# Optimization experiments

Measured on AMD Instinct MI355X. Metric: run time of the kernel, lower is better.

Reference implementation:

```python
import jax, jax.numpy as jnp
import numpy as np

# ---- static config (mirrors SRNNConfig) ----
N = 2048          # num_units
N_E = N // 2      # excitatory
N_I = N - N_E     # inhibitory
N_A = 3           # n_a_E = n_a_I (SFA timescales per neuron)
H = 0.04
UNFOLDS = 6
DT = H / UNFOLDS
IN_SIZE = 512
B = 512
STATE_SIZE = N_E * N_A + N_I * N_A + N_E + N_I + N  # 10240
SPARSITY = 0.5


def inv_softplus(x):
    return float(np.log(np.expm1(x)))


def piecewise_sigmoid(x, S_a=0.9, S_c=0.0):
    """Bounded [0,1] activation: linear center, quadratic edges (matches torch source)."""
    a = S_a / 2.0
    c = S_c
    k = 0.5 / (1.0 - 2.0 * a)  # = 5.0 for S_a=0.9
    x1 = c + a - 1.0
    x2 = c - a
    x3 = c + a
    x4 = c + 1.0 - a
    quad_rise = k * (x - x1) * (x - x1)
    linear = x - c + 0.5
    quad_cap = 1.0 - k * (x - x4) * (x - x4)
    out = jnp.where(x < x1, jnp.zeros_like(x), quad_rise)
    out = jnp.where(x >= x2, linear, out)
    out = jnp.where(x > x3, quad_cap, out)
    out = jnp.where(x > x4, jnp.ones_like(x), out)
    return out


def setup_inputs() -> dict:
    key = jax.random.key(0)
    ks = jax.random.split(key, 6)
    f32 = jnp.float32
    W_raw = (jax.random.normal(ks[0], (N, N)) * np.sqrt(2.0 / N)).astype(f32)
    sparsity_mask = (jax.random.uniform(ks[1], (N, N)) > SPARSITY).astype(f32)
    W_raw = W_raw * sparsity_mask  # W_init masked as in __init__
    W_in = (jax.random.normal(ks[2], (N, IN_SIZE)) * 0.1).astype(f32)
    a_0 = jnp.full((N,), 0.35, f32)
    log_tau_d = jnp.full((1,), inv_softplus(0.1), f32)
    log_tau_a_E_lo = jnp.full((1, 1), inv_softplus(0.25), f32)
    log_tau_a_E_hi = jnp.full((1, 1), inv_softplus(10.0), f32)
    log_c_E = jnp.full((1, N_A), -3.0, f32)
    c_0_E = jnp.zeros((1, N_A), f32)
    log_tau_a_I_lo = jnp.full((1, 1), inv_softplus(0.25), f32)
    log_tau_a_I_hi = jnp.full((1, 1), inv_softplus(10.0), f32)
    log_c_I = jnp.full((1, N_A), -3.0, f32)
    c_0_I = jnp.zeros((1, N_A), f32)
    log_tau_b_rec_E = jnp.full((1,), inv_softplus(1.0), f32)
    log_tau_b_rel_E = jnp.full((1,), inv_softplus(0.25), f32)
    log_tau_b_rec_I = jnp.full((1,), inv_softplus(1.0), f32)
    log_tau_b_rel_I = jnp.full((1,), inv_softplus(0.25), f32)
    u = jax.random.normal(ks[3], (B, IN_SIZE), f32)
    state = jax.random.normal(ks[4], (B, STATE_SIZE), f32) * 0.1
    return {
        "W_raw": W_raw, "W_in": W_in, "sparsity_mask": sparsity_mask, "a_0": a_0,
        "log_tau_d": log_tau_d,
        "log_tau_a_E_lo": log_tau_a_E_lo, "log_tau_a_E_hi": log_tau_a_E_hi,
        "log_c_E": log_c_E, "c_0_E": c_0_E,
        "log_tau_a_I_lo": log_tau_a_I_lo, "log_tau_a_I_hi": log_tau_a_I_hi,
        "log_c_I": log_c_I, "c_0_I": c_0_I,
        "log_tau_b_rec_E": log_tau_b_rec_E, "log_tau_b_rel_E": log_tau_b_rel_E,
        "log_tau_b_rec_I": log_tau_b_rec_I, "log_tau_b_rel_I": log_tau_b_rel_I,
        "u": u, "state": state,
    }


def reference(W_raw, W_in, sparsity_mask, a_0, log_tau_d,
              log_tau_a_E_lo, log_tau_a_E_hi, log_c_E, c_0_E,
              log_tau_a_I_lo, log_tau_a_I_hi, log_c_I, c_0_I,
              log_tau_b_rec_E, log_tau_b_rel_E, log_tau_b_rec_I, log_tau_b_rel_I,
              u, state):
    sp = jax.nn.softplus
    # ---- unpack flat state: [a_E, a_I, b_E, b_I, x] ----
    i = 0
    a_E = state[:, i:i + N_E * N_A].reshape(-1, N_E, N_A); i += N_E * N_A
    a_I = state[:, i:i + N_I * N_A].reshape(-1, N_I, N_A); i += N_I * N_A
    b_E = state[:, i:i + N_E]; i += N_E
    b_I = state[:, i:i + N_I]; i += N_I
    x = state[:, i:i + N]

    # ---- effective weights (Dale's law: E cols +, I cols -) + sparsity ----
    W_pos = sp(W_raw)
    sign = jnp.concatenate([jnp.ones((N_E,), W_raw.dtype), -jnp.ones((N_I,), W_raw.dtype)])
    W_eff = W_pos * sign[None, :] * sparsity_mask  # (N, N)

    # ---- time constants / coefficients ----
    tau_d = sp(log_tau_d)                              # (1,)
    t = jnp.linspace(0.0, 1.0, N_A).astype(x.dtype)
    tau_a_E = sp(log_tau_a_E_lo) + (sp(log_tau_a_E_hi) - sp(log_tau_a_E_lo)) * t  # (1, N_A)
    tau_a_I = sp(log_tau_a_I_lo) + (sp(log_tau_a_I_hi) - sp(log_tau_a_I_lo)) * t
    c_E = sp(log_c_E)                                  # (1, N_A)
    c_I = sp(log_c_I)
    tau_b_rec_E = sp(log_tau_b_rec_E); tau_b_rel_E = sp(log_tau_b_rel_E)
    tau_b_rec_I = sp(log_tau_b_rec_I); tau_b_rel_I = sp(log_tau_b_rel_I)

    I_ext = u @ W_in.T + a_0[None, :]                  # (B, N), constant over sub-steps

    g_x = DT / tau_d                                   # (1,)
    g_aE = DT / tau_a_E[None]                          # (1, 1, N_A)
    g_aI = DT / tau_a_I[None]

    for _ in range(UNFOLDS):
        # adaptation-shifted membrane potential
        x_eff_E = x[:, :N_E] - (a_E * c_E[None]).sum(-1)   # (B, N_E)
        x_eff_I = x[:, N_E:] - (a_I * c_I[None]).sum(-1)   # (B, N_I)
        r = piecewise_sigmoid(jnp.concatenate([x_eff_E, x_eff_I], axis=-1))  # (B, N)
        r_E, r_I = r[:, :N_E], r[:, N_E:]
        # synaptic depression gates the transmitted rates
        r_dep = jnp.concatenate([b_E * r_E, b_I * r_I], axis=-1)
        I_syn = r_dep @ W_eff.T + I_ext                    # (B, N)
        # ---- semi-implicit Euler sub-step ----
        x = (x + g_x * I_syn) / (1.0 + g_x)
        a_E = (a_E + g_aE * (r_E[:, :, None] + c_0_E[None])) / (1.0 + g_aE)
        a_I = (a_I + g_aI * (r_I[:, :, None] + c_0_I[None])) / (1.0 + g_aI)
        b_E = (b_E + DT / tau_b_rec_E) / (1.0 + DT / tau_b_rec_E + DT * r_E / tau_b_rel_E)
        b_I = (b_I + DT / tau_b_rec_I) / (1.0 + DT / tau_b_rec_I + DT * r_I / tau_b_rel_I)

    batch = state.shape[0]
    new_state = jnp.concatenate(
        [a_E.reshape(batch, -1), a_I.reshape(batch, -1), b_E, b_I, x], axis=-1)
    return new_state
```

## Files before the change

### kernel.cpp

```cpp
#include <hip/hip_runtime.h>
#include <math.h>

#define N_TOT 2048
#define NE    1024
#define BATCH 512
#define IN_SZ 512
#define SS    10240
#define AI_OFF 3072
#define BE_OFF 6144
#define BI_OFF 7168
#define X_OFF  8192

typedef __attribute__((ext_vector_type(8))) short bf16x8;
typedef __attribute__((ext_vector_type(4))) float f32x4;


__device__ __forceinline__ float sp_f(float x) {
    return fmaxf(x, 0.f) + log1pf(expf(-fabsf(x)));
}

__device__ __forceinline__ float psig(float x) {
    if (x >= -0.45f) {
        if (x <= 0.45f) return x + 0.5f;
        if (x > 0.55f)  return 1.f;
        float d = x - 0.55f;
        return 1.f - 5.f * d * d;
    }
    if (x < -0.55f) return 0.f;
    float d = x + 0.55f;
    return 5.f * d * d;
}

__device__ __forceinline__ ushort f2bf(float f) {
    unsigned u = __float_as_uint(f);
    unsigned r = (u + 0x7fffu + ((u >> 16) & 1u)) >> 16;
    return (ushort)r;
}

__device__ __forceinline__ void gload16(const void* g, void* l) {
    __builtin_amdgcn_global_load_lds(
        (const __attribute__((address_space(1))) void*)g,
        (__attribute__((address_space(3))) void*)l, 16, 0, 0);
}

__global__ void k_params(const float* ltd, const float* loE, const float* hiE,
                         const float* lcE, const float* c0E,
                         const float* loI, const float* hiI,
                         const float* lcI, const float* c0I,
                         const float* recE, const float* relE,
                         const float* recI, const float* relI,
                         float* __restrict__ P) {
    if (threadIdx.x == 0 && blockIdx.x == 0) {
        const float DTf = (float)(0.04 / 6.0);
        float gx = DTf / sp_f(ltd[0]);
        P[0] = gx;
        P[29] = 1.f / (1.f + gx);
        float sElo = sp_f(loE[0]), sEhi = sp_f(hiE[0]);
        float sIlo = sp_f(loI[0]), sIhi = sp_f(hiI[0]);
        for (int j = 0; j < 3; ++j) {
            float t = 0.5f * (float)j;
            float gE = DTf / (sElo + (sEhi - sElo) * t);
            float gI = DTf / (sIlo + (sIhi - sIlo) * t);
            P[1 + j] = gE;  P[23 + j] = 1.f / (1.f + gE);
            P[4 + j] = gI;  P[26 + j] = 1.f / (1.f + gI);
            P[7 + j]  = sp_f(lcE[j]);
            P[10 + j] = sp_f(lcI[j]);
            P[13 + j] = c0E[j];
            P[16 + j] = c0I[j];
        }
        P[19] = DTf / sp_f(recE[0]);
        P[20] = DTf / sp_f(relE[0]);
        P[21] = DTf / sp_f(recI[0]);
        P[22] = DTf / sp_f(relI[0]);
    }
}

__global__ __launch_bounds__(256) void k_weff(const float* __restrict__ Wr,
                                              const float* __restrict__ mask,
                                              ushort* __restrict__ We) {
    int i = blockIdx.x * 256 + threadIdx.x;
    float4 w = ((const float4*)Wr)[i];
    float4 m = ((const float4*)mask)[i];
    int col = (i * 4) & (N_TOT - 1);
    float s = (col < NE) ? 1.f : -1.f;
    ushort4 o;
    o.x = f2bf(sp_f(w.x) * m.x * s);
    o.y = f2bf(sp_f(w.y) * m.y * s);
    o.z = f2bf(sp_f(w.z) * m.z * s);
    o.w = f2bf(sp_f(w.w) * m.w * s);
    ((ushort4*)We)[i] = o;
}

__global__ __launch_bounds__(256) void k_cvt(const float* __restrict__ in,
                                             ushort* __restrict__ out) {
    int i = blockIdx.x * 256 + threadIdx.x;
    float4 v = ((const float4*)in)[i];
    ushort4 o;
    o.x = f2bf(v.x); o.y = f2bf(v.y); o.z = f2bf(v.z); o.w = f2bf(v.w);
    ((ushort4*)out)[i] = o;
}

__global__ __launch_bounds__(256) void k_r_first(const float* __restrict__ st,
                                                 const float* __restrict__ P,
                                                 float* __restrict__ r_ws,
                                                 ushort* __restrict__ rdep) {
    int idx = blockIdx.x * 256 + threadIdx.x;
    int m = idx >> 11, n = idx & (N_TOT - 1);
    const float* row = st + (size_t)m * SS;
    bool isE = n < NE;
    int na = isE ? n : n - NE;
    const float* a = row + (isE ? 0 : AI_OFF) + 3 * na;
    const float* c = P + (isE ? 7 : 10);
    float x = row[X_OFF + n];
    float xeff = x - (a[0] * c[0] + a[1] * c[1] + a[2] * c[2]);
    float r = psig(xeff);
    float bb = row[isE ? (BE_OFF + n) : (BI_OFF + na)];
    r_ws[idx] = r;
    rdep[idx] = f2bf(bb * r);
}

template<int EPI, bool CALC_R>
__global__ __launch_bounds__(256)
void mgemm(const ushort* __restrict__ A, const ushort* __restrict__ Bt, int K,
           const float* __restrict__ a0,
           const float* __restrict__ Iext,
           float* __restrict__ outIext,
           float* __restrict__ stateOut,
           const float* __restrict__ P,
           float* __restrict__ r_ws,
           ushort* __restrict__ rdep_out) {
    __shared__ __align__(16) ushort lds[2][2][64 * 32];
    const int tid = threadIdx.x;
    const int bm = blockIdx.y * 64;
    const int bn = blockIdx.x * 64;
    const int wv = tid >> 6;
    const int lane = tid & 63;
    const int wr = wv >> 1, wc = wv & 1;

    const int srow = tid >> 2;
    const int sc = tid & 3;
    const int gk = (sc ^ ((srow >> 1) & 3)) * 8;
    const ushort* gA = A + (size_t)(bm + srow) * K + gk;
    const ushort* gB = Bt + (size_t)(bn + srow) * K + gk;

    int aoff[2], boff[2];
    {
        const int kc = lane >> 4;
        const int rr = lane & 15;
#pragma unroll
        for (int i = 0; i < 2; ++i) {
            int r = wr * 32 + i * 16 + rr;
            aoff[i] = r * 64 + ((kc ^ ((r >> 1) & 3)) << 4);
        }
#pragma unroll
        for (int j = 0; j < 2; ++j) {
            int r = wc * 32 + j * 16 + rr;
            boff[j] = r * 64 + ((kc ^ ((r >> 1) & 3)) << 4);
        }
    }

    f32x4 acc[2][2];
#pragma unroll
    for (int i = 0; i < 2; ++i)
#pragma unroll
        for (int j = 0; j < 2; ++j)
            acc[i][j] = f32x4{0.f, 0.f, 0.f, 0.f};

    gload16(gA, (char*)&lds[0][0][0] + wv * 1024);
    gload16(gB, (char*)&lds[0][1][0] + wv * 1024);
    __syncthreads();

    const int nsteps = K >> 5;
    int cur = 0;
    for (int s = 0; s < nsteps; ++s) {
        if (s + 1 < nsteps) {
            gload16(gA + (s + 1) * 32, (char*)&lds[cur ^ 1][0][0] + wv * 1024);
            gload16(gB + (s + 1) * 32, (char*)&lds[cur ^ 1][1][0] + wv * 1024);
        }
        const char* At = (const char*)&lds[cur][0][0];
        const char* Bl = (const char*)&lds[cur][1][0];
        bf16x8 af0 = *(const bf16x8*)(At + aoff[0]);
        bf16x8 af1 = *(const bf16x8*)(At + aoff[1]);
        bf16x8 bg0 = *(const bf16x8*)(Bl + boff[0]);
        bf16x8 bg1 = *(const bf16x8*)(Bl + boff[1]);
        acc[0][0] = __builtin_amdgcn_mfma_f32_16x16x32_bf16(af0, bg0, acc[0][0], 0, 0, 0);
        acc[0][1] = __builtin_amdgcn_mfma_f32_16x16x32_bf16(af0, bg1, acc[0][1], 0, 0, 0);
        acc[1][0] = __builtin_amdgcn_mfma_f32_16x16x32_bf16(af1, bg0, acc[1][0], 0, 0, 0);
        acc[1][1] = __builtin_amdgcn_mfma_f32_16x16x32_bf16(af1, bg1, acc[1][1], 0, 0, 0);
        __syncthreads();
        cur ^= 1;
    }

    if (EPI == 0) {
#pragma unroll
        for (int i = 0; i < 2; ++i) {
#pragma unroll
            for (int j = 0; j < 2; ++j) {
                int m0 = bm + wr * 32 + i * 16 + (lane >> 4) * 4;
                int n = bn + wc * 32 + j * 16 + (lane & 15);
                float av = a0[n];
#pragma unroll
                for (int q = 0; q < 4; ++q)
                    outIext[(m0 + q) * N_TOT + n] = acc[i][j][q] + av;
            }
        }
    } else {
        const float gx = P[0];
        const float inv1gx = P[29];
#pragma unroll
        for (int i = 0; i < 2; ++i) {
#pragma unroll
            for (int j = 0; j < 2; ++j) {
                int m0 = bm + wr * 32 + i * 16 + (lane >> 4) * 4;
                int n = bn + wc * 32 + j * 16 + (lane & 15);
                bool isE = n < NE;
                int na = isE ? n : n - NE;
                const float* ga = P + (isE ? 1 : 4);
                const float* iga = P + (isE ? 23 : 26);
                const float* c0 = P + (isE ? 13 : 16);
                const float* cc = P + (isE ? 7 : 10);
                float kbrec = isE ? P[19] : P[21];
                float kbrel = isE ? P[20] : P[22];
                int aofs = (isE ? 0 : AI_OFF) + 3 * na;
                int bofs = isE ? (BE_OFF + n) : (BI_OFF + na);
#pragma unroll
                for (int q = 0; q < 4; ++q) {
                    int m = m0 + q;
                    float* row = stateOut + (size_t)m * SS;
                    int idx = m * N_TOT + n;
                    float Isyn = acc[i][j][q] + Iext[idx];
                    float x = row[X_OFF + n];
                    float xn = (x + gx * Isyn) * inv1gx;
                    row[X_OFF + n] = xn;

                    float r = r_ws[idx];
                    float* a = row + aofs;
                    float av0 = (a[0] + ga[0] * (r + c0[0])) * iga[0];
                    float av1 = (a[1] + ga[1] * (r + c0[1])) * iga[1];
                    float av2 = (a[2] + ga[2] * (r + c0[2])) * iga[2];
                    a[0] = av0; a[1] = av1; a[2] = av2;

                    float bb = row[bofs];
                    bb = (bb + kbrec) / (1.f + kbrec + kbrel * r);
                    row[bofs] = bb;

                    if (CALC_R) {
                        float xeff = xn - (av0 * cc[0] + av1 * cc[1] + av2 * cc[2]);
                        float rn = psig(xeff);
                        r_ws[idx] = rn;
                        rdep_out[idx] = f2bf(bb * rn);
                    }
                }
            }
        }
    }
}

extern "C" void kernel_launch(void* const* d_in, const int* in_sizes, int n_in,
                              void* d_out, int out_size, void* d_ws, size_t ws_size,
                              hipStream_t stream) {
    const float* W_raw = (const float*)d_in[0];
    const float* W_in  = (const float*)d_in[1];
    const float* mask  = (const float*)d_in[2];
    const float* a_0   = (const float*)d_in[3];
    const float* ltd   = (const float*)d_in[4];
    const float* loE   = (const float*)d_in[5];
    const float* hiE   = (const float*)d_in[6];
    const float* lcE   = (const float*)d_in[7];
    const float* c0E   = (const float*)d_in[8];
    const float* loI   = (const float*)d_in[9];
    const float* hiI   = (const float*)d_in[10];
    const float* lcI   = (const float*)d_in[11];
    const float* c0I   = (const float*)d_in[12];
    const float* recE  = (const float*)d_in[13];
    const float* relE  = (const float*)d_in[14];
    const float* recI  = (const float*)d_in[15];
    const float* relI  = (const float*)d_in[16];
    const float* u     = (const float*)d_in[17];
    const float* state = (const float*)d_in[18];
    float* out = (float*)d_out;
    char* wsb = (char*)d_ws;

    ushort* We     = (ushort*)(wsb);
    float*  Iext   = (float*)(wsb + (8u << 20));
    float*  r_ws   = (float*)(wsb + (12u << 20));
    ushort* rdep0  = (ushort*)(wsb + (16u << 20));
    ushort* rdep1  = (ushort*)(wsb + (18u << 20));
    ushort* u_bf   = (ushort*)(wsb + (20u << 20));
    ushort* win_bf = (ushort*)(wsb + (21u << 20));
    float*  P      = (float*)(wsb + (23u << 20));

    hipMemcpyAsync(out, state, (size_t)BATCH * SS * sizeof(float),
                   hipMemcpyDeviceToDevice, stream);

    k_params<<<1, 64, 0, stream>>>(ltd, loE, hiE, lcE, c0E, loI, hiI, lcI, c0I,
                                   recE, relE, recI, relI, P);

    k_weff<<<(N_TOT * N_TOT / 4) / 256, 256, 0, stream>>>(W_raw, mask, We);
    k_cvt<<<(BATCH * IN_SZ / 4) / 256, 256, 0, stream>>>(u, u_bf);
    k_cvt<<<(N_TOT * IN_SZ / 4) / 256, 256, 0, stream>>>(W_in, win_bf);

    mgemm<0, false><<<dim3(N_TOT / 64, BATCH / 64), 256, 0, stream>>>(
        u_bf, win_bf, IN_SZ, a_0, nullptr, Iext, nullptr, nullptr, nullptr, nullptr);

    k_r_first<<<(BATCH * N_TOT) / 256, 256, 0, stream>>>(out, P, r_ws, rdep0);

    ushort* rbufs[2] = {rdep0, rdep1};
    for (int t = 0; t < 6; ++t) {
        ushort* rin  = rbufs[t & 1];
        ushort* rout = rbufs[(t + 1) & 1];
        if (t < 5)
            mgemm<1, true><<<dim3(N_TOT / 64, BATCH / 64), 256, 0, stream>>>(
                rin, We, N_TOT, nullptr, Iext, nullptr, out, P, r_ws, rout);
        else
            mgemm<1, false><<<dim3(N_TOT / 64, BATCH / 64), 256, 0, stream>>>(
                rin, We, N_TOT, nullptr, Iext, nullptr, out, P, r_ws, nullptr);
    }
}
```

Before: 374.9 us.

## Fuse input GEMM and all unfold steps into one persistent kernel with grid barrier

Replaces the separate input-projection GEMM, first-rate kernel and six per-step GEMM launches with one persistent kernel of 256 blocks. The blocks synchronise between sub-steps through an atomic global barrier. Each thread keeps its slice of x, a, b, r and I_ext in registers across all steps, and writes the state only once at the end. This drops the full-state device copy and the global Iext and r_ws round-trips. The K tile grows to 128 with a 512-thread block, at the cost of spin-barrier latency and a requirement that all 256 blocks are co-resident.

```diff
diff --git a/kernel.cpp b/kernel.cpp
--- a/kernel.cpp
+++ b/kernel.cpp
@@ -10,6 +10,8 @@
 #define BE_OFF 6144
 #define BI_OFF 7168
 #define X_OFF  8192
+#define NBLK  256
+#define LDS_B_OFF 16384
 
 typedef __attribute__((ext_vector_type(8))) short bf16x8;
 typedef __attribute__((ext_vector_type(4))) float f32x4;
@@ -43,14 +45,37 @@
         (__attribute__((address_space(3))) void*)l, 16, 0, 0);
 }
 
+__device__ __forceinline__ void gbar(unsigned* bar) {
+    __threadfence();
+    __syncthreads();
+    if (threadIdx.x == 0) {
+        unsigned* cnt = bar;
+        unsigned* gen = bar + 1;
+        unsigned g = __hip_atomic_load(gen, __ATOMIC_RELAXED, __HIP_MEMORY_SCOPE_AGENT);
+        unsigned a = __hip_atomic_fetch_add(cnt, 1u, __ATOMIC_ACQ_REL, __HIP_MEMORY_SCOPE_AGENT);
+        if (a == NBLK - 1) {
+            __hip_atomic_store(cnt, 0u, __ATOMIC_RELAXED, __HIP_MEMORY_SCOPE_AGENT);
+            __hip_atomic_fetch_add(gen, 1u, __ATOMIC_RELEASE, __HIP_MEMORY_SCOPE_AGENT);
+        } else {
+            while (__hip_atomic_load(gen, __ATOMIC_ACQUIRE, __HIP_MEMORY_SCOPE_AGENT) == g) {
+                __builtin_amdgcn_s_sleep(2);
+            }
+        }
+    }
+    __syncthreads();
+    __threadfence();
+}
+
 __global__ void k_params(const float* ltd, const float* loE, const float* hiE,
                          const float* lcE, const float* c0E,
                          const float* loI, const float* hiI,
                          const float* lcI, const float* c0I,
                          const float* recE, const float* relE,
                          const float* recI, const float* relI,
-                         float* __restrict__ P) {
+                         float* __restrict__ P, unsigned* __restrict__ bar) {
     if (threadIdx.x == 0 && blockIdx.x == 0) {
+        bar[0] = 0u;
+        bar[1] = 0u;
         const float DTf = (float)(0.04 / 6.0);
         float gx = DTf / sp_f(ltd[0]);
         P[0] = gx;
@@ -100,158 +125,181 @@
     ((ushort4*)out)[i] = o;
 }
 
-__global__ __launch_bounds__(256) void k_r_first(const float* __restrict__ st,
-                                                 const float* __restrict__ P,
-                                                 float* __restrict__ r_ws,
-                                                 ushort* __restrict__ rdep) {
-    int idx = blockIdx.x * 256 + threadIdx.x;
-    int m = idx >> 11, n = idx & (N_TOT - 1);
-    const float* row = st + (size_t)m * SS;
-    bool isE = n < NE;
-    int na = isE ? n : n - NE;
-    const float* a = row + (isE ? 0 : AI_OFF) + 3 * na;
-    const float* c = P + (isE ? 7 : 10);
-    float x = row[X_OFF + n];
-    float xeff = x - (a[0] * c[0] + a[1] * c[1] + a[2] * c[2]);
-    float r = psig(xeff);
-    float bb = row[isE ? (BE_OFF + n) : (BI_OFF + na)];
-    r_ws[idx] = r;
-    rdep[idx] = f2bf(bb * r);
-}
-
-template<int EPI, bool CALC_R>
-__global__ __launch_bounds__(256)
-void mgemm(const ushort* __restrict__ A, const ushort* __restrict__ Bt, int K,
-           const float* __restrict__ a0,
-           const float* __restrict__ Iext,
-           float* __restrict__ outIext,
-           float* __restrict__ stateOut,
-           const float* __restrict__ P,
-           float* __restrict__ r_ws,
-           ushort* __restrict__ rdep_out) {
-    __shared__ __align__(16) ushort lds[2][2][64 * 32];
-    const int tid = threadIdx.x;
-    const int bm = blockIdx.y * 64;
-    const int bn = blockIdx.x * 64;
-    const int wv = tid >> 6;
+__global__ __launch_bounds__(512, 2)
+void kfused(const ushort* __restrict__ We,
+            const ushort* __restrict__ u_bf,
+            const ushort* __restrict__ win_bf,
+            const float* __restrict__ a0,
+            const float* __restrict__ P,
+            const float* __restrict__ state_in,
+            float* __restrict__ state_out,
+            ushort* __restrict__ rdep0,
+            ushort* __restrict__ rdep1,
+            unsigned* __restrict__ bar) {
+    __shared__ __align__(16) ushort lds[2][16384];
+    const int tid  = threadIdx.x;
     const int lane = tid & 63;
-    const int wr = wv >> 1, wc = wv & 1;
-
-    const int srow = tid >> 2;
-    const int sc = tid & 3;
-    const int gk = (sc ^ ((srow >> 1) & 3)) * 8;
-    const ushort* gA = A + (size_t)(bm + srow) * K + gk;
-    const ushort* gB = Bt + (size_t)(bn + srow) * K + gk;
-
-    int aoff[2], boff[2];
+    const int wv   = tid >> 6;
+    const int wr   = wv >> 1;
+    const int wc   = wv & 1;
+    const int bn   = blockIdx.x * 64;
+    const int bm   = blockIdx.y * 64;
+
+    const int srow = tid >> 4;
+    const int sch  = tid & 15;
+    const int sgc  = sch ^ (srow & 7);
+
+    const int kc = lane >> 4, rr = lane & 15;
+    const int ar = wr * 16 + rr;
+    int aO[4], bO0[4], bO1[4];
     {
-        const int kc = lane >> 4;
-        const int rr = lane & 15;
-#pragma unroll
-        for (int i = 0; i < 2; ++i) {
-            int r = wr * 32 + i * 16 + rr;
-            aoff[i] = r * 64 + ((kc ^ ((r >> 1) & 3)) << 4);
-        }
+        const int br0 = wc * 32 + rr;
+        const int br1 = wc * 32 + 16 + rr;
+#pragma unroll
+        for (int s = 0; s < 4; ++s) {
+            aO[s]  = ar * 256 + (((s * 4 + kc) ^ (ar & 7)) << 4);
+            bO0[s] = LDS_B_OFF + br0 * 256 + (((s * 4 + kc) ^ (br0 & 7)) << 4);
+            bO1[s] = LDS_B_OFF + br1 * 256 + (((s * 4 + kc) ^ (br1 & 7)) << 4);
+        }
+    }
+
+    auto stage = [&](int buf, const ushort* A, const ushort* Bt, int K, int k0) {
+        char* Ld = (char*)&lds[buf][0];
+        const ushort* Ap  = A  + (size_t)(bm + srow) * K + k0 + sgc * 8;
+        const ushort* Ap2 = A  + (size_t)(bm + srow + 32) * K + k0 + sgc * 8;
+        const ushort* Bp  = Bt + (size_t)(bn + srow) * K + k0 + sgc * 8;
+        const ushort* Bp2 = Bt + (size_t)(bn + srow + 32) * K + k0 + sgc * 8;
+        gload16(Ap,  Ld + tid * 16);
+        gload16(Ap2, Ld + tid * 16 + 8192);
+        gload16(Bp,  Ld + LDS_B_OFF + tid * 16);
+        gload16(Bp2, Ld + LDS_B_OFF + tid * 16 + 8192);
+    };
+    auto compute = [&](int buf, f32x4* acc) {
+        const char* Ld = (const char*)&lds[buf][0];
+#pragma unroll
+        for (int s = 0; s < 4; ++s) {
+            bf16x8 af = *(const bf16x8*)(Ld + aO[s]);
+            bf16x8 b0 = *(const bf16x8*)(Ld + bO0[s]);
+            bf16x8 b1 = *(const bf16x8*)(Ld + bO1[s]);
+            acc[0] = __builtin_amdgcn_mfma_f32_16x16x32_bf16(af, b0, acc[0], 0, 0, 0);
+            acc[1] = __builtin_amdgcn_mfma_f32_16x16x32_bf16(af, b1, acc[1], 0, 0, 0);
+        }
+    };
+    auto gemmK = [&](const ushort* A, const ushort* Bt, int K, f32x4* acc) {
+        const int nkt = K >> 7;
+        stage(0, A, Bt, K, 0);
+        __syncthreads();
+        for (int kt = 0; kt < nkt; ++kt) {
+            int cur = kt & 1;
+            if (kt + 1 < nkt) stage(cur ^ 1, A, Bt, K, (kt + 1) << 7);
+            compute(cur, acc);
+            __syncthreads();
+        }
+    };
+
+    const float gx = P[0], inv1gx = P[29];
+    const int mbase = bm + wr * 16 + (lane >> 4) * 4;
+    int nj[2], aofs[2], bofs[2];
+    float ga[2][3], iga[2][3], c0v[2][3], ccv[2][3], kbrecv[2], kbrelv[2];
+#pragma unroll
+    for (int j = 0; j < 2; ++j) {
+        int n = bn + wc * 32 + j * 16 + (lane & 15);
+        nj[j] = n;
+        bool isE = n < NE;
+        int na = isE ? n : n - NE;
+#pragma unroll
+        for (int c = 0; c < 3; ++c) {
+            ga[j][c]  = P[(isE ? 1 : 4) + c];
+            iga[j][c] = P[(isE ? 23 : 26) + c];
+            c0v[j][c] = P[(isE ? 13 : 16) + c];
+            ccv[j][c] = P[(isE ? 7 : 10) + c];
+        }
+        kbrecv[j] = isE ? P[19] : P[21];
+        kbrelv[j] = isE ? P[20] : P[22];
+        aofs[j] = (isE ? 0 : AI_OFF) + 3 * na;
+        bofs[j] = isE ? (BE_OFF + n) : (BI_OFF + na);
+    }
+
+    f32x4 acc[2];
+    acc[0] = f32x4{0.f, 0.f, 0.f, 0.f};
+    acc[1] = f32x4{0.f, 0.f, 0.f, 0.f};
+    gemmK(u_bf, win_bf, IN_SZ, acc);
+
+    float iext[2][4], xs[2][4], as[2][4][3], bs[2][4], rs[2][4];
+#pragma unroll
+    for (int j = 0; j < 2; ++j) {
+        float a0v = a0[nj[j]];
+#pragma unroll
+        for (int q = 0; q < 4; ++q) iext[j][q] = acc[j][q] + a0v;
+    }
+
+#pragma unroll
+    for (int j = 0; j < 2; ++j) {
+#pragma unroll
+        for (int q = 0; q < 4; ++q) {
+            int m = mbase + q;
+            const float* row = state_in + (size_t)m * SS;
+            float xv  = row[X_OFF + nj[j]];
+            float av0 = row[aofs[j] + 0];
+            float av1 = row[aofs[j] + 1];
+            float av2 = row[aofs[j] + 2];
+            float bv  = row[bofs[j]];
+            xs[j][q] = xv;
+            as[j][q][0] = av0; as[j][q][1] = av1; as[j][q][2] = av2;
+            bs[j][q] = bv;
+            float xeff = xv - (av0 * ccv[j][0] + av1 * ccv[j][1] + av2 * ccv[j][2]);
+            float rv = psig(xeff);
+            rs[j][q] = rv;
+            rdep0[(size_t)m * N_TOT + nj[j]] = f2bf(bv * rv);
+        }
+    }
+    gbar(bar);
+
+    ushort* rin  = rdep0;
+    ushort* rout = rdep1;
+    for (int t = 0; t < 6; ++t) {
+        acc[0] = f32x4{0.f, 0.f, 0.f, 0.f};
+        acc[1] = f32x4{0.f, 0.f, 0.f, 0.f};
+        gemmK(rin, We, N_TOT, acc);
 #pragma unroll
         for (int j = 0; j < 2; ++j) {
-            int r = wc * 32 + j * 16 + rr;
-            boff[j] = r * 64 + ((kc ^ ((r >> 1) & 3)) << 4);
-        }
-    }
-
-    f32x4 acc[2][2];
-#pragma unroll
-    for (int i = 0; i < 2; ++i)
-#pragma unroll
-        for (int j = 0; j < 2; ++j)
-            acc[i][j] = f32x4{0.f, 0.f, 0.f, 0.f};
-
-    gload16(gA, (char*)&lds[0][0][0] + wv * 1024);
-    gload16(gB, (char*)&lds[0][1][0] + wv * 1024);
-    __syncthreads();
-
-    const int nsteps = K >> 5;
-    int cur = 0;
-    for (int s = 0; s < nsteps; ++s) {
-        if (s + 1 < nsteps) {
-            gload16(gA + (s + 1) * 32, (char*)&lds[cur ^ 1][0][0] + wv * 1024);
-            gload16(gB + (s + 1) * 32, (char*)&lds[cur ^ 1][1][0] + wv * 1024);
-        }
-        const char* At = (const char*)&lds[cur][0][0];
-        const char* Bl = (const char*)&lds[cur][1][0];
-        bf16x8 af0 = *(const bf16x8*)(At + aoff[0]);
-        bf16x8 af1 = *(const bf16x8*)(At + aoff[1]);
-        bf16x8 bg0 = *(const bf16x8*)(Bl + boff[0]);
-        bf16x8 bg1 = *(const bf16x8*)(Bl + boff[1]);
-        acc[0][0] = __builtin_amdgcn_mfma_f32_16x16x32_bf16(af0, bg0, acc[0][0], 0, 0, 0);
-        acc[0][1] = __builtin_amdgcn_mfma_f32_16x16x32_bf16(af0, bg1, acc[0][1], 0, 0, 0);
-        acc[1][0] = __builtin_amdgcn_mfma_f32_16x16x32_bf16(af1, bg0, acc[1][0], 0, 0, 0);
-        acc[1][1] = __builtin_amdgcn_mfma_f32_16x16x32_bf16(af1, bg1, acc[1][1], 0, 0, 0);
-        __syncthreads();
-        cur ^= 1;
-    }
-
-    if (EPI == 0) {
-#pragma unroll
-        for (int i = 0; i < 2; ++i) {
-#pragma unroll
-            for (int j = 0; j < 2; ++j) {
-                int m0 = bm + wr * 32 + i * 16 + (lane >> 4) * 4;
-                int n = bn + wc * 32 + j * 16 + (lane & 15);
-                float av = a0[n];
-#pragma unroll
-                for (int q = 0; q < 4; ++q)
-                    outIext[(m0 + q) * N_TOT + n] = acc[i][j][q] + av;
-            }
-        }
-    } else {
-        const float gx = P[0];
-        const float inv1gx = P[29];
-#pragma unroll
-        for (int i = 0; i < 2; ++i) {
-#pragma unroll
-            for (int j = 0; j < 2; ++j) {
-                int m0 = bm + wr * 32 + i * 16 + (lane >> 4) * 4;
-                int n = bn + wc * 32 + j * 16 + (lane & 15);
-                bool isE = n < NE;
-                int na = isE ? n : n - NE;
-                const float* ga = P + (isE ? 1 : 4);
-                const float* iga = P + (isE ? 23 : 26);
-                const float* c0 = P + (isE ? 13 : 16);
-                const float* cc = P + (isE ? 7 : 10);
-                float kbrec = isE ? P[19] : P[21];
-                float kbrel = isE ? P[20] : P[22];
-                int aofs = (isE ? 0 : AI_OFF) + 3 * na;
-                int bofs = isE ? (BE_OFF + n) : (BI_OFF + na);
-#pragma unroll
-                for (int q = 0; q < 4; ++q) {
-                    int m = m0 + q;
-                    float* row = stateOut + (size_t)m * SS;
-                    int idx = m * N_TOT + n;
-                    float Isyn = acc[i][j][q] + Iext[idx];
-                    float x = row[X_OFF + n];
-                    float xn = (x + gx * Isyn) * inv1gx;
-                    row[X_OFF + n] = xn;
-
-                    float r = r_ws[idx];
-                    float* a = row + aofs;
-                    float av0 = (a[0] + ga[0] * (r + c0[0])) * iga[0];
-                    float av1 = (a[1] + ga[1] * (r + c0[1])) * iga[1];
-                    float av2 = (a[2] + ga[2] * (r + c0[2])) * iga[2];
-                    a[0] = av0; a[1] = av1; a[2] = av2;
-
-                    float bb = row[bofs];
-                    bb = (bb + kbrec) / (1.f + kbrec + kbrel * r);
-                    row[bofs] = bb;
-
-                    if (CALC_R) {
-                        float xeff = xn - (av0 * cc[0] + av1 * cc[1] + av2 * cc[2]);
-                        float rn = psig(xeff);
-                        r_ws[idx] = rn;
-                        rdep_out[idx] = f2bf(bb * rn);
-                    }
+#pragma unroll
+            for (int q = 0; q < 4; ++q) {
+                float Isyn = acc[j][q] + iext[j][q];
+                float xn = (xs[j][q] + gx * Isyn) * inv1gx;
+                xs[j][q] = xn;
+                float rv = rs[j][q];
+                float an0 = (as[j][q][0] + ga[j][0] * (rv + c0v[j][0])) * iga[j][0];
+                float an1 = (as[j][q][1] + ga[j][1] * (rv + c0v[j][1])) * iga[j][1];
+                float an2 = (as[j][q][2] + ga[j][2] * (rv + c0v[j][2])) * iga[j][2];
+                as[j][q][0] = an0; as[j][q][1] = an1; as[j][q][2] = an2;
+                float bnv = (bs[j][q] + kbrecv[j]) /
+                            (1.f + kbrecv[j] + kbrelv[j] * rv);
+                bs[j][q] = bnv;
+                if (t < 5) {
+                    float xeff = xn - (an0 * ccv[j][0] + an1 * ccv[j][1] + an2 * ccv[j][2]);
+                    float rn = psig(xeff);
+                    rs[j][q] = rn;
+                    rout[(size_t)(mbase + q) * N_TOT + nj[j]] = f2bf(bnv * rn);
                 }
             }
+        }
+        if (t < 5) {
+            gbar(bar);
+            ushort* tmp = rin; rin = rout; rout = tmp;
+        }
+    }
+
+#pragma unroll
+    for (int j = 0; j < 2; ++j) {
+#pragma unroll
+        for (int q = 0; q < 4; ++q) {
+            float* row = state_out + (size_t)(mbase + q) * SS;
+            row[X_OFF + nj[j]] = xs[j][q];
+            row[aofs[j] + 0] = as[j][q][0];
+            row[aofs[j] + 1] = as[j][q][1];
+            row[aofs[j] + 2] = as[j][q][2];
+            row[bofs[j]] = bs[j][q];
         }
     }
 }
@@ -281,39 +329,21 @@
     float* out = (float*)d_out;
     char* wsb = (char*)d_ws;
 
-    ushort* We     = (ushort*)(wsb);
-    float*  Iext   = (float*)(wsb + (8u << 20));
-    float*  r_ws   = (float*)(wsb + (12u << 20));
-    ushort* rdep0  = (ushort*)(wsb + (16u << 20));
-    ushort* rdep1  = (ushort*)(wsb + (18u << 20));
-    ushort* u_bf   = (ushort*)(wsb + (20u << 20));
-    ushort* win_bf = (ushort*)(wsb + (21u << 20));
-    float*  P      = (float*)(wsb + (23u << 20));
-
-    hipMemcpyAsync(out, state, (size_t)BATCH * SS * sizeof(float),
-                   hipMemcpyDeviceToDevice, stream);
+    ushort*   We     = (ushort*)(wsb);
+    ushort*   rdep0  = (ushort*)(wsb + (8u << 20));
+    ushort*   rdep1  = (ushort*)(wsb + (10u << 20));
+    ushort*   u_bf   = (ushort*)(wsb + (12u << 20));
+    ushort*   win_bf = (ushort*)(wsb + (13u << 20));
+    unsigned* bar    = (unsigned*)(wsb + (15u << 20));
+    float*    P      = (float*)(wsb + (15u << 20) + 256);
 
     k_params<<<1, 64, 0, stream>>>(ltd, loE, hiE, lcE, c0E, loI, hiI, lcI, c0I,
-                                   recE, relE, recI, relI, P);
+                                   recE, relE, recI, relI, P, bar);
 
     k_weff<<<(N_TOT * N_TOT / 4) / 256, 256, 0, stream>>>(W_raw, mask, We);
     k_cvt<<<(BATCH * IN_SZ / 4) / 256, 256, 0, stream>>>(u, u_bf);
     k_cvt<<<(N_TOT * IN_SZ / 4) / 256, 256, 0, stream>>>(W_in, win_bf);
 
-    mgemm<0, false><<<dim3(N_TOT / 64, BATCH / 64), 256, 0, stream>>>(
-        u_bf, win_bf, IN_SZ, a_0, nullptr, Iext, nullptr, nullptr, nullptr, nullptr);
-
-    k_r_first<<<(BATCH * N_TOT) / 256, 256, 0, stream>>>(out, P, r_ws, rdep0);
-
-    ushort* rbufs[2] = {rdep0, rdep1};
-    for (int t = 0; t < 6; ++t) {
-        ushort* rin  = rbufs[t & 1];
-        ushort* rout = rbufs[(t + 1) & 1];
-        if (t < 5)
-            mgemm<1, true><<<dim3(N_TOT / 64, BATCH / 64), 256, 0, stream>>>(
-                rin, We, N_TOT, nullptr, Iext, nullptr, out, P, r_ws, rout);
-        else
-            mgemm<1, false><<<dim3(N_TOT / 64, BATCH / 64), 256, 0, stream>>>(
-                rin, We, N_TOT, nullptr, Iext, nullptr, out, P, r_ws, nullptr);
-    }
-}
+    kfused<<<dim3(32, 8), 512, 0, stream>>>(We, u_bf, win_bf, a_0, P,
+                                            state, out, rdep0, rdep1, bar);
+}
```

Result: slower. 841.1 us (+124.3%).
